# Kernel optimization log

Measured on AMD Instinct MI355X. Metric: run time of the kernel, lower is better.

## Reference

```python
import jax, jax.numpy as jnp
import numpy as np

EPS = 0.5  # energy-relaxation learning rate (epsilon in __init__)


def rho(s):
    return jnp.clip(s, 0.0, 1.0)


def setup_inputs() -> dict:
    key = jax.random.key(0)
    k_x, k_w1, k_w2 = jax.random.split(key, 3)
    B, I, H, O = 8192, 1024, 128, 1000
    x = jax.random.uniform(k_x, (B, I), dtype=jnp.float32)
    hidden0 = jnp.zeros((B, H), dtype=jnp.float32)
    output0 = jnp.zeros((B, O), dtype=jnp.float32)
    b_in = jnp.zeros((I,), dtype=jnp.float32)
    b_h = jnp.zeros((H,), dtype=jnp.float32)
    b_o = jnp.zeros((O,), dtype=jnp.float32)
    # xavier_uniform: U(-a, a), a = sqrt(6 / (fan_in + fan_out))
    a1 = np.sqrt(6.0 / (I + H)).astype(np.float32)
    a2 = np.sqrt(6.0 / (H + O)).astype(np.float32)
    W1 = jax.random.uniform(k_w1, (I, H), minval=-a1, maxval=a1, dtype=jnp.float32)
    W2 = jax.random.uniform(k_w2, (H, O), minval=-a2, maxval=a2, dtype=jnp.float32)
    return {"x": x, "hidden0": hidden0, "output0": output0,
            "b_in": b_in, "b_h": b_h, "b_o": b_o,
            "W1": W1, "W2": W2, "n_iterations": 30}


def reference(x, hidden0, output0, b_in, b_h, b_o, W1, W2, n_iterations):
    # Hopfield-style energy summed over the batch (beta=0 / free phase):
    # E = 0.5*sum rho(s)^2 - sum rho(s).b - sum rho(pre) W rho(post)
    def energy(h, o):
        rx, rh, ro = rho(x), rho(h), rho(o)
        sq = 0.5 * ((rx * rx).sum() + (rh * rh).sum() + (ro * ro).sum())
        lin = -(rx @ b_in).sum() - (rh @ b_h).sum() - (ro @ b_o).sum()
        quad = -jnp.einsum('bi,ih,bh->', rx, W1, rh) \
               - jnp.einsum('bh,ho,bo->', rh, W2, ro)
        return sq + lin + quad

    grad_e = jax.grad(energy, argnums=(0, 1))

    def step(carry, _):
        h, o = carry
        gh, go = grad_e(h, o)
        h = jnp.clip(h - EPS * gh, 0.0, 1.0)
        o = jnp.clip(o - EPS * go, 0.0, 1.0)
        return (h, o), None

    (h, o), _ = jax.lax.scan(step, (hidden0, output0), None, length=n_iterations)
    return jax.nn.log_softmax(o, axis=1)
```

## Files before the change

kernel.cpp:

```cpp
#include <hip/hip_runtime.h>
#include <hip/hip_bf16.h>

typedef __bf16 bf16_t;
typedef __bf16 bf16x4_t __attribute__((ext_vector_type(4)));
typedef __bf16 bf16x8 __attribute__((ext_vector_type(8)));
typedef float f32x16 __attribute__((ext_vector_type(16)));

#define EPS 0.5f
#define MFMA32(a, b, c) __builtin_amdgcn_mfma_f32_32x32x16_bf16(a, b, c, 0, 0, 0)

__global__ __launch_bounds__(256) void prep_weights(
    const float* __restrict__ W1, const float* __restrict__ W2,
    bf16_t* __restrict__ W1t, bf16_t* __restrict__ W2B, bf16_t* __restrict__ W2T) {
  int idx = blockIdx.x * 256 + threadIdx.x;
  if (idx < 131072) {
    { int j = idx >> 10, i = idx & 1023; W1t[idx] = (bf16_t)W1[i * 128 + j]; }
    { int e = idx & 7, l = (idx >> 3) & 63, s = (idx >> 9) & 63, jt = idx >> 15;
      int j = jt * 32 + (l & 31), k = s * 16 + (l >> 5) * 8 + e;
      W2B[idx] = (bf16_t)((k < 1000) ? W2[j * 1000 + k] : 0.f); }
    { int e = idx & 7, l = (idx >> 3) & 63, js = (idx >> 9) & 7, kt = idx >> 12;
      int k = kt * 32 + (l & 31), j = js * 16 + (l >> 5) * 8 + e;
      W2T[idx] = (bf16_t)((k < 1000) ? W2[j * 1000 + k] : 0.f); }
  }
}

__global__ __launch_bounds__(256) void gemm_A(
    const float* __restrict__ x, const bf16_t* __restrict__ W1t,
    float* __restrict__ A) {
  int lane = threadIdx.x & 63, w = threadIdx.x >> 6;
  int row0 = blockIdx.x * 64;
  int mt = w & 1, np = (w >> 1) * 2;
  f32x16 acc0 = {}, acc1 = {};
  int ar = row0 + mt * 32 + (lane & 31);
  int kg = (lane >> 5) * 8;
  const float* xrow = x + (size_t)ar * 1024 + kg;
  const bf16_t* b0 = W1t + ((np * 32 + (lane & 31)) << 10) + kg;
  const bf16_t* b1 = W1t + (((np + 1) * 32 + (lane & 31)) << 10) + kg;
#pragma unroll 4
  for (int ks = 0; ks < 64; ++ks) {
    float xv[8];
    *(float4*)&xv[0] = *(const float4*)(xrow + ks * 16);
    *(float4*)&xv[4] = *(const float4*)(xrow + ks * 16 + 4);
    bf16x8 a;
#pragma unroll
    for (int i = 0; i < 8; ++i) a[i] = (bf16_t)xv[i];
    bf16x8 f0 = *(const bf16x8*)(b0 + ks * 16);
    bf16x8 f1 = *(const bf16x8*)(b1 + ks * 16);
    acc0 = MFMA32(a, f0, acc0);
    acc1 = MFMA32(a, f1, acc1);
  }
#pragma unroll
  for (int reg = 0; reg < 16; ++reg) {
    int r = mt * 32 + (reg & 3) + 8 * (reg >> 2) + 4 * (lane >> 5);
    A[(size_t)(row0 + r) * 128 + np * 32 + (lane & 31)] = acc0[reg];
    A[(size_t)(row0 + r) * 128 + (np + 1) * 32 + (lane & 31)] = acc1[reg];
  }
}

__device__ __forceinline__ bf16x4_t upd4(bf16x4_t v4, const float* u, bool& chgd) {
  bf16x4_t n4;
#pragma unroll
  for (int r = 0; r < 4; ++r) {
    float v = (float)v4[r];
    float g = __builtin_fmaf(v, v, -v);
    float st = (g == 0.f) ? 0.25f : 0.5f;
    float n = __builtin_fmaf(-st, v - u[r], v);
    n4[r] = (bf16_t)__builtin_amdgcn_fmed3f(n, 0.f, 1.f);
  }
  unsigned long long ov, nv;
  __builtin_memcpy(&ov, &v4, 8);
  __builtin_memcpy(&nv, &n4, 8);
  chgd |= (ov != nv);
  return n4;
}

__global__ __launch_bounds__(1024, 4) void eqprop(
    const float* __restrict__ h0, const float* __restrict__ o0,
    const float* __restrict__ b_h, const float* __restrict__ b_o,
    const float* __restrict__ A, const bf16_t* __restrict__ W2B,
    const bf16_t* __restrict__ W2T, const int* __restrict__ nit,
    float* __restrict__ out) {
  __shared__ __align__(16) char o_raw[131072];
  __shared__ __align__(16) char h_raw[16384];
  __shared__ float bo_lds[1024];
  __shared__ int chg[32];

  const int tid = threadIdx.x, lane = tid & 63, w = tid >> 6;
  const int lo = lane & 31, hi = lane >> 5;
  const int row0 = blockIdx.x * 32;

  for (int idx = tid; idx < 32768; idx += 1024) {
    int b = idx >> 10, k = idx & 1023;
    float v = (k < 1000) ? o0[(size_t)(row0 + b) * 1000 + k] : 0.f;
    int ad = ((k >> 4) << 10) + ((((k >> 3) & 1) << 5) + b) * 16 + ((k & 7) << 1);
    *(bf16_t*)(o_raw + ad) = (bf16_t)v;
  }
  for (int idx = tid; idx < 4096; idx += 1024) {
    int b = idx >> 7, j = idx & 127;
    int ad = ((j >> 4) << 10) + ((((j >> 3) & 1) << 5) + b) * 16 + ((j & 7) << 1);
    *(bf16_t*)(h_raw + ad) = (bf16_t)h0[(size_t)(row0 + b) * 128 + j];
  }
  bo_lds[tid] = (tid < 1000) ? b_o[tid] : 0.f;
  if (tid < 32) chg[tid] = 0;

  const int T = nit[0];
  int p = 0;
  __syncthreads();

  if (w < 4) {
    const int jt = w;
    const bf16_t* WB = W2B + (size_t)jt * 32768 + lane * 8;
#define CW(s) (*(const bf16x8*)(WB + (s) * 512))
    bf16x8 wres[16];
#pragma unroll
    for (int s = 0; s < 16; ++s) wres[s] = CW(s);
    const char* obase = o_raw + lane * 16;

    for (int t = 0; t < T; ++t) {
      const char* obP = obase + (p << 16);
#define OF(s) (*(const bf16x8*)(obP + (s) * 1024))
      f32x16 acc = {};
      __builtin_amdgcn_s_setprio(1);
#pragma unroll
      for (int s = 0; s < 16; ++s) acc = MFMA32(wres[s], OF(s), acc);
      __builtin_amdgcn_s_setprio(0);
      bf16x8 cs0[4], cs1[4];
      cs0[0] = CW(16); cs0[1] = CW(17); cs0[2] = CW(18); cs0[3] = CW(19);
#pragma unroll 1
      for (int c = 0; c < 12; ++c) {
        const int s0 = 16 + c * 4;
        if ((c & 1) == 0) {
          if (c < 11) {
            cs1[0] = CW(s0 + 4); cs1[1] = CW(s0 + 5);
            cs1[2] = CW(s0 + 6); cs1[3] = CW(s0 + 7);
          }
          __builtin_amdgcn_s_setprio(1);
          acc = MFMA32(cs0[0], OF(s0 + 0), acc);
          acc = MFMA32(cs0[1], OF(s0 + 1), acc);
          acc = MFMA32(cs0[2], OF(s0 + 2), acc);
          acc = MFMA32(cs0[3], OF(s0 + 3), acc);
          __builtin_amdgcn_s_setprio(0);
        } else {
          if (c < 11) {
            cs0[0] = CW(s0 + 4); cs0[1] = CW(s0 + 5);
            cs0[2] = CW(s0 + 6); cs0[3] = CW(s0 + 7);
          }
          __builtin_amdgcn_s_setprio(1);
          acc = MFMA32(cs1[0], OF(s0 + 0), acc);
          acc = MFMA32(cs1[1], OF(s0 + 1), acc);
          acc = MFMA32(cs1[2], OF(s0 + 2), acc);
          acc = MFMA32(cs1[3], OF(s0 + 3), acc);
          __builtin_amdgcn_s_setprio(0);
        }
      }
      const char* hrd = h_raw + (p << 13) + lo * 16 + hi * 8;
      char* hwr = h_raw + ((p ^ 1) << 13) + lo * 16 + hi * 8;
      bool chgd = false;
#pragma unroll
      for (int q = 0; q < 4; ++q) {
        const int jb = jt * 32 + q * 8 + 4 * hi;
        const int boff = (jt * 2 + (q >> 1)) * 1024 + (q & 1) * 512;
        float av[4], bh[4], u[4];
        *(float4*)av = *(const float4*)(A + (size_t)(row0 + lo) * 128 + jb);
        *(float4*)bh = *(const float4*)(b_h + jb);
#pragma unroll
        for (int r = 0; r < 4; ++r) u[r] = av[r] + bh[r] + acc[q * 4 + r];
        bf16x4_t v4 = *(const bf16x4_t*)(hrd + boff);
        *(bf16x4_t*)(hwr + boff) = upd4(v4, u, chgd);
      }
      if (__ballot(chgd) && lane == 0) atomicOr(&chg[t & 31], 1);
      __syncthreads();
      p ^= 1;
      if (chg[t & 31] == 0) break;
    }
  } else {
    const int wd = w - 4;
    const int kt0 = (wd < 8) ? wd * 3 : 24 + (wd - 8) * 2;
    const int nkt = (wd < 8) ? 3 : 2;
    const bf16_t* WT = W2T + (size_t)kt0 * 4096 + lane * 8;
#define DW(f) (*(const bf16x8*)(WT + (f) * 512))
    bf16x8 wres[8];
#pragma unroll
    for (int f = 0; f < 8; ++f) wres[f] = DW(f);
    const char* hbase = h_raw + lane * 16;
    const char* obase = o_raw + lo * 16 + hi * 8;

    for (int t = 0; t < T; ++t) {
      const char* hbP = hbase + (p << 13);
      bf16x8 hf[8];
#pragma unroll
      for (int js = 0; js < 8; ++js)
        hf[js] = *(const bf16x8*)(hbP + js * 1024);
      const char* ord = obase + (p << 16);
      char* owr = o_raw + lo * 16 + hi * 8 + ((p ^ 1) << 16);
      bool chgd = false;

#pragma unroll 1
      for (int kl = 0; kl < nkt; ++kl) {
        const int kt = kt0 + kl;
        f32x16 acc = {};
        if (kl == 0) {
          __builtin_amdgcn_s_setprio(1);
#pragma unroll
          for (int js = 0; js < 8; ++js) acc = MFMA32(wres[js], hf[js], acc);
          __builtin_amdgcn_s_setprio(0);
        } else {
          bf16x8 s0 = DW(kl * 8 + 0), s1 = DW(kl * 8 + 1);
          bf16x8 s2 = DW(kl * 8 + 2), s3 = DW(kl * 8 + 3);
          bf16x8 s4 = DW(kl * 8 + 4), s5 = DW(kl * 8 + 5);
          bf16x8 s6 = DW(kl * 8 + 6), s7 = DW(kl * 8 + 7);
          __builtin_amdgcn_s_setprio(1);
          acc = MFMA32(s0, hf[0], acc);
          acc = MFMA32(s1, hf[1], acc);
          acc = MFMA32(s2, hf[2], acc);
          acc = MFMA32(s3, hf[3], acc);
          acc = MFMA32(s4, hf[4], acc);
          acc = MFMA32(s5, hf[5], acc);
          acc = MFMA32(s6, hf[6], acc);
          acc = MFMA32(s7, hf[7], acc);
          __builtin_amdgcn_s_setprio(0);
        }
#pragma unroll
        for (int q = 0; q < 4; ++q) {
          const int boff = (kt * 2 + (q >> 1)) * 1024 + (q & 1) * 512;
          float bo4[4], u[4];
          *(float4*)bo4 = *(const float4*)(bo_lds + kt * 32 + q * 8 + 4 * hi);
#pragma unroll
          for (int r = 0; r < 4; ++r) u[r] = bo4[r] + acc[q * 4 + r];
          bf16x4_t v4 = *(const bf16x4_t*)(ord + boff);
          *(bf16x4_t*)(owr + boff) = upd4(v4, u, chgd);
        }
      }
      if (__ballot(chgd) && lane == 0) atomicOr(&chg[t & 31], 1);
      __syncthreads();
      p ^= 1;
      if (chg[t & 31] == 0) break;
    }
  }
  __syncthreads();

  const char* of = o_raw + (p << 16);
  for (int row = w * 2; row < w * 2 + 2; ++row) {
    float m = -1e30f;
    for (int k = lane; k < 1000; k += 64) {
      int ad = ((k >> 4) << 10) + ((((k >> 3) & 1) << 5) + row) * 16 + ((k & 7) << 1);
      m = fmaxf(m, (float)*(const bf16_t*)(of + ad));
    }
#pragma unroll
    for (int s = 32; s > 0; s >>= 1) m = fmaxf(m, __shfl_xor(m, s));
    float sum = 0.f;
    for (int k = lane; k < 1000; k += 64) {
      int ad = ((k >> 4) << 10) + ((((k >> 3) & 1) << 5) + row) * 16 + ((k & 7) << 1);
      sum += expf((float)*(const bf16_t*)(of + ad) - m);
    }
#pragma unroll
    for (int s = 32; s > 0; s >>= 1) sum += __shfl_xor(sum, s);
    float lse = m + logf(sum);
    for (int k = lane; k < 1000; k += 64) {
      int ad = ((k >> 4) << 10) + ((((k >> 3) & 1) << 5) + row) * 16 + ((k & 7) << 1);
      out[(size_t)(row0 + row) * 1000 + k] =
          (float)*(const bf16_t*)(of + ad) - lse;
    }
  }
}

extern "C" void kernel_launch(void* const* d_in, const int* in_sizes, int n_in,
                              void* d_out, int out_size, void* d_ws, size_t ws_size,
                              hipStream_t stream) {
  const float* x   = (const float*)d_in[0];
  const float* h0  = (const float*)d_in[1];
  const float* o0  = (const float*)d_in[2];
  const float* b_h = (const float*)d_in[4];
  const float* b_o = (const float*)d_in[5];
  const float* W1  = (const float*)d_in[6];
  const float* W2  = (const float*)d_in[7];
  const int*   nit = (const int*)d_in[8];
  float* out = (float*)d_out;

  char* ws = (char*)d_ws;
  float*  A   = (float*)ws;
  bf16_t* W1t = (bf16_t*)(ws + 4194304);
  bf16_t* W2B = (bf16_t*)(ws + 4194304 + 262144);
  bf16_t* W2T = (bf16_t*)(ws + 4194304 + 524288);

  prep_weights<<<512, 256, 0, stream>>>(W1, W2, W1t, W2B, W2T);
  gemm_A<<<128, 256, 0, stream>>>(x, W1t, A);
  eqprop<<<256, 1024, 0, stream>>>(h0, o0, b_h, b_o, A, W2B, W2T, nit, out);
}
```

Measured before the change: 267.6 us.

## Drop convergence early-exit, remove setprio, prefetch W2T fragments across k-tiles

```diff
diff --git a/kernel.cpp b/kernel.cpp
--- a/kernel.cpp
+++ b/kernel.cpp
@@ -57,7 +57,7 @@
   }
 }
 
-__device__ __forceinline__ bf16x4_t upd4(bf16x4_t v4, const float* u, bool& chgd) {
+__device__ __forceinline__ bf16x4_t upd4(bf16x4_t v4, const float* u) {
   bf16x4_t n4;
 #pragma unroll
   for (int r = 0; r < 4; ++r) {
@@ -67,10 +67,6 @@
     float n = __builtin_fmaf(-st, v - u[r], v);
     n4[r] = (bf16_t)__builtin_amdgcn_fmed3f(n, 0.f, 1.f);
   }
-  unsigned long long ov, nv;
-  __builtin_memcpy(&ov, &v4, 8);
-  __builtin_memcpy(&nv, &n4, 8);
-  chgd |= (ov != nv);
   return n4;
 }
 
@@ -83,7 +79,6 @@
   __shared__ __align__(16) char o_raw[131072];
   __shared__ __align__(16) char h_raw[16384];
   __shared__ float bo_lds[1024];
-  __shared__ int chg[32];
 
   const int tid = threadIdx.x, lane = tid & 63, w = tid >> 6;
   const int lo = lane & 31, hi = lane >> 5;
@@ -101,7 +96,6 @@
     *(bf16_t*)(h_raw + ad) = (bf16_t)h0[(size_t)(row0 + b) * 128 + j];
   }
   bo_lds[tid] = (tid < 1000) ? b_o[tid] : 0.f;
-  if (tid < 32) chg[tid] = 0;
 
   const int T = nit[0];
   int p = 0;
@@ -120,10 +114,8 @@
       const char* obP = obase + (p << 16);
 #define OF(s) (*(const bf16x8*)(obP + (s) * 1024))
       f32x16 acc = {};
-      __builtin_amdgcn_s_setprio(1);
 #pragma unroll
       for (int s = 0; s < 16; ++s) acc = MFMA32(wres[s], OF(s), acc);
-      __builtin_amdgcn_s_setprio(0);
       bf16x8 cs0[4], cs1[4];
       cs0[0] = CW(16); cs0[1] = CW(17); cs0[2] = CW(18); cs0[3] = CW(19);
 #pragma unroll 1
@@ -134,28 +126,23 @@
             cs1[0] = CW(s0 + 4); cs1[1] = CW(s0 + 5);
             cs1[2] = CW(s0 + 6); cs1[3] = CW(s0 + 7);
           }
-          __builtin_amdgcn_s_setprio(1);
           acc = MFMA32(cs0[0], OF(s0 + 0), acc);
           acc = MFMA32(cs0[1], OF(s0 + 1), acc);
           acc = MFMA32(cs0[2], OF(s0 + 2), acc);
           acc = MFMA32(cs0[3], OF(s0 + 3), acc);
-          __builtin_amdgcn_s_setprio(0);
         } else {
           if (c < 11) {
             cs0[0] = CW(s0 + 4); cs0[1] = CW(s0 + 5);
             cs0[2] = CW(s0 + 6); cs0[3] = CW(s0 + 7);
           }
-          __builtin_amdgcn_s_setprio(1);
           acc = MFMA32(cs1[0], OF(s0 + 0), acc);
           acc = MFMA32(cs1[1], OF(s0 + 1), acc);
           acc = MFMA32(cs1[2], OF(s0 + 2), acc);
           acc = MFMA32(cs1[3], OF(s0 + 3), acc);
-          __builtin_amdgcn_s_setprio(0);
         }
       }
       const char* hrd = h_raw + (p << 13) + lo * 16 + hi * 8;
       char* hwr = h_raw + ((p ^ 1) << 13) + lo * 16 + hi * 8;
-      bool chgd = false;
 #pragma unroll
       for (int q = 0; q < 4; ++q) {
         const int jb = jt * 32 + q * 8 + 4 * hi;
@@ -166,12 +153,10 @@
 #pragma unroll
         for (int r = 0; r < 4; ++r) u[r] = av[r] + bh[r] + acc[q * 4 + r];
         bf16x4_t v4 = *(const bf16x4_t*)(hrd + boff);
-        *(bf16x4_t*)(hwr + boff) = upd4(v4, u, chgd);
-      }
-      if (__ballot(chgd) && lane == 0) atomicOr(&chg[t & 31], 1);
+        *(bf16x4_t*)(hwr + boff) = upd4(v4, u);
+      }
       __syncthreads();
       p ^= 1;
-      if (chg[t & 31] == 0) break;
     }
   } else {
     const int wd = w - 4;
@@ -193,32 +178,40 @@
         hf[js] = *(const bf16x8*)(hbP + js * 1024);
       const char* ord = obase + (p << 16);
       char* owr = o_raw + lo * 16 + hi * 8 + ((p ^ 1) << 16);
-      bool chgd = false;
+
+      bf16x8 sw[8];
+#pragma unroll
+      for (int js = 0; js < 8; ++js) sw[js] = DW(8 + js);
+
+      f32x16 acc = {};
+#pragma unroll
+      for (int js = 0; js < 8; ++js) acc = MFMA32(wres[js], hf[js], acc);
+#pragma unroll
+      for (int q = 0; q < 4; ++q) {
+        const int boff = (kt0 * 2 + (q >> 1)) * 1024 + (q & 1) * 512;
+        float bo4[4], u[4];
+        *(float4*)bo4 = *(const float4*)(bo_lds + kt0 * 32 + q * 8 + 4 * hi);
+#pragma unroll
+        for (int r = 0; r < 4; ++r) u[r] = bo4[r] + acc[q * 4 + r];
+        bf16x4_t v4 = *(const bf16x4_t*)(ord + boff);
+        *(bf16x4_t*)(owr + boff) = upd4(v4, u);
+      }
 
 #pragma unroll 1
-      for (int kl = 0; kl < nkt; ++kl) {
+      for (int kl = 1; kl < nkt; ++kl) {
         const int kt = kt0 + kl;
-        f32x16 acc = {};
-        if (kl == 0) {
-          __builtin_amdgcn_s_setprio(1);
-#pragma unroll
-          for (int js = 0; js < 8; ++js) acc = MFMA32(wres[js], hf[js], acc);
-          __builtin_amdgcn_s_setprio(0);
-        } else {
-          bf16x8 s0 = DW(kl * 8 + 0), s1 = DW(kl * 8 + 1);
-          bf16x8 s2 = DW(kl * 8 + 2), s3 = DW(kl * 8 + 3);
-          bf16x8 s4 = DW(kl * 8 + 4), s5 = DW(kl * 8 + 5);
-          bf16x8 s6 = DW(kl * 8 + 6), s7 = DW(kl * 8 + 7);
-          __builtin_amdgcn_s_setprio(1);
-          acc = MFMA32(s0, hf[0], acc);
-          acc = MFMA32(s1, hf[1], acc);
-          acc = MFMA32(s2, hf[2], acc);
-          acc = MFMA32(s3, hf[3], acc);
-          acc = MFMA32(s4, hf[4], acc);
-          acc = MFMA32(s5, hf[5], acc);
-          acc = MFMA32(s6, hf[6], acc);
-          acc = MFMA32(s7, hf[7], acc);
-          __builtin_amdgcn_s_setprio(0);
+        f32x16 a2 = {};
+        a2 = MFMA32(sw[0], hf[0], a2);
+        a2 = MFMA32(sw[1], hf[1], a2);
+        a2 = MFMA32(sw[2], hf[2], a2);
+        a2 = MFMA32(sw[3], hf[3], a2);
+        a2 = MFMA32(sw[4], hf[4], a2);
+        a2 = MFMA32(sw[5], hf[5], a2);
+        a2 = MFMA32(sw[6], hf[6], a2);
+        a2 = MFMA32(sw[7], hf[7], a2);
+        if (kl + 1 < nkt) {
+#pragma unroll
+          for (int js = 0; js < 8; ++js) sw[js] = DW((kl + 1) * 8 + js);
         }
 #pragma unroll
         for (int q = 0; q < 4; ++q) {
@@ -226,15 +219,13 @@
           float bo4[4], u[4];
           *(float4*)bo4 = *(const float4*)(bo_lds + kt * 32 + q * 8 + 4 * hi);
 #pragma unroll
-          for (int r = 0; r < 4; ++r) u[r] = bo4[r] + acc[q * 4 + r];
+          for (int r = 0; r < 4; ++r) u[r] = bo4[r] + a2[q * 4 + r];
           bf16x4_t v4 = *(const bf16x4_t*)(ord + boff);
-          *(bf16x4_t*)(owr + boff) = upd4(v4, u, chgd);
+          *(bf16x4_t*)(owr + boff) = upd4(v4, u);
         }
       }
-      if (__ballot(chgd) && lane == 0) atomicOr(&chg[t & 31], 1);
       __syncthreads();
       p ^= 1;
-      if (chg[t & 31] == 0) break;
     }
   }
   __syncthreads();
```

New measurement: 437.9 us. 63.6% more time.
